# Optimization experiments

Measured on AMD Instinct MI355X. Metric: run time of the kernel, lower is better.

Reference implementation:

```python
import jax, jax.numpy as jnp
import numpy as np

DIM = 384
NUM_HEADS = 12
WS = 8            # window_size
SS = 4            # shift_size
HEAD_DIM = DIM // NUM_HEADS
SCALE = HEAD_DIM ** -0.5
N = WS * WS       # tokens per window
EPS = 1e-5
MLP_HIDDEN = 4 * DIM

# relative position index (static, matches torch buffer construction)
_coords = np.stack(np.meshgrid(np.arange(WS), np.arange(WS), indexing='ij')).reshape(2, -1)
_rel = (_coords[:, :, None] - _coords[:, None, :]).transpose(1, 2, 0)  # [N,N,2]
_rel[..., 0] += WS - 1
_rel[..., 1] += WS - 1
_rel[..., 0] *= 2 * WS - 1
RPI = jnp.asarray(_rel.sum(-1))  # [N,N] int


def layer_norm(x, g, b):
    m = x.mean(-1, keepdims=True)
    v = ((x - m) ** 2).mean(-1, keepdims=True)
    return (x - m) / jnp.sqrt(v + EPS) * g + b


def window_partition(x):
    B, Hh, Ww, C = x.shape
    x = x.reshape(B, Hh // WS, WS, Ww // WS, WS, C).transpose(0, 1, 3, 2, 4, 5)
    return x.reshape(-1, WS, WS, C)


def window_reverse(w, Hh, Ww):
    B = w.shape[0] // ((Hh // WS) * (Ww // WS))
    x = w.reshape(B, Hh // WS, Ww // WS, WS, WS, -1).transpose(0, 1, 3, 2, 4, 5)
    return x.reshape(B, Hh, Ww, -1)


def attention_mask(Hp, Wp):
    # region id along each axis: 0 = [0, Hp-WS), 1 = [Hp-WS, Hp-SS), 2 = [Hp-SS, Hp)
    h_id = np.zeros(Hp, np.int32); h_id[Hp - WS:Hp - SS] = 1; h_id[Hp - SS:] = 2
    w_id = np.zeros(Wp, np.int32); w_id[Wp - WS:Wp - SS] = 1; w_id[Wp - SS:] = 2
    cnt = h_id[:, None] * 3 + w_id[None, :]                      # [Hp, Wp]
    img = jnp.asarray(cnt, jnp.float32).reshape(1, Hp, Wp, 1)
    mw = window_partition(img).reshape(-1, N)                    # [nW, N]
    am = mw[:, None, :] - mw[:, :, None]                         # [nW, N, N]
    return jnp.where(am != 0, jnp.float32(-100.0), jnp.float32(0.0))


def setup_inputs() -> dict:
    key = jax.random.key(0)
    ks = jax.random.split(key, 8)
    B, H, W = 32, 64, 64
    std = 0.02
    return {
        'x': jax.random.normal(ks[0], (B, H * W, DIM), jnp.float32),
        'qkv_w': jax.random.normal(ks[1], (DIM, 3 * DIM), jnp.float32) * std,
        'qkv_b': jnp.zeros((3 * DIM,), jnp.float32),
        'proj_w': jax.random.normal(ks[2], (DIM, DIM), jnp.float32) * std,
        'proj_b': jnp.zeros((DIM,), jnp.float32),
        'rpb_table': jax.random.normal(ks[3], ((2 * WS - 1) * (2 * WS - 1), NUM_HEADS), jnp.float32) * std,
        'n1_g': jnp.ones((DIM,), jnp.float32), 'n1_b': jnp.zeros((DIM,), jnp.float32),
        'n2_g': jnp.ones((DIM,), jnp.float32), 'n2_b': jnp.zeros((DIM,), jnp.float32),
        'fc1_w': jax.random.normal(ks[4], (DIM, MLP_HIDDEN), jnp.float32) * std,
        'fc1_b': jnp.zeros((MLP_HIDDEN,), jnp.float32),
        'fc2_w': jax.random.normal(ks[5], (MLP_HIDDEN, DIM), jnp.float32) * std,
        'fc2_b': jnp.zeros((DIM,), jnp.float32),
        'H': 64, 'W': 64,
    }


def reference(x, qkv_w, qkv_b, proj_w, proj_b, rpb_table, n1_g, n1_b, n2_g, n2_b,
              fc1_w, fc1_b, fc2_w, fc2_b, H, W):
    B, L, C = x.shape
    shortcut = x
    h = layer_norm(x, n1_g, n1_b).reshape(B, H, W, C)
    pad_r = (WS - W % WS) % WS
    pad_b = (WS - H % WS) % WS
    if pad_r or pad_b:
        h = jnp.pad(h, ((0, 0), (0, pad_b), (0, pad_r), (0, 0)))
    Hp, Wp = H + pad_b, W + pad_r
    shifted = jnp.roll(h, shift=(-SS, -SS), axis=(1, 2))
    xw = window_partition(shifted).reshape(-1, N, C)             # [B_, N, C]
    B_ = xw.shape[0]

    qkv = (xw @ qkv_w + qkv_b).reshape(B_, N, 3, NUM_HEADS, HEAD_DIM)
    q = qkv[:, :, 0].transpose(0, 2, 1, 3) * SCALE               # [B_, h, N, d]
    k = qkv[:, :, 1].transpose(0, 2, 1, 3)
    v = qkv[:, :, 2].transpose(0, 2, 1, 3)

    attn = jnp.einsum('bhnd,bhmd->bhnm', q, k)                   # [B_, h, N, N]
    bias = rpb_table[RPI].transpose(2, 0, 1)                     # [h, N, N]
    attn = attn + bias[None]

    mask = attention_mask(Hp, Wp)                                # [nW, N, N]
    nW = mask.shape[0]
    attn = attn.reshape(B_ // nW, nW, NUM_HEADS, N, N) + mask[None, :, None]
    attn = jax.nn.softmax(attn.reshape(B_, NUM_HEADS, N, N), axis=-1)

    out = jnp.einsum('bhnm,bhmd->bhnd', attn, v)
    out = out.transpose(0, 2, 1, 3).reshape(B_, N, C)
    out = out @ proj_w + proj_b

    out = window_reverse(out.reshape(-1, WS, WS, C), Hp, Wp)
    out = jnp.roll(out, shift=(SS, SS), axis=(1, 2))
    out = out[:, :H, :W, :].reshape(B, H * W, C)

    x = shortcut + out
    h2 = layer_norm(x, n2_g, n2_b)
    mlp = jax.nn.gelu(h2 @ fc1_w + fc1_b, approximate=False) @ fc2_w + fc2_b
    return x + mlp
```

## Files before the change

### kernel.cpp

```cpp
#include <hip/hip_runtime.h>
#include <math.h>


#define ROWS_TOTAL 131072
#define NWIN_TOTAL 2048

typedef __attribute__((ext_vector_type(8))) __bf16 bf16x8;
typedef __attribute__((ext_vector_type(4))) float f32x4;
typedef __attribute__((ext_vector_type(8))) unsigned short ushort8;

__device__ __forceinline__ unsigned short f2bf(float f) {
  unsigned u = __builtin_bit_cast(unsigned, f);
  u = (u + 0x7fffu + ((u >> 16) & 1u)) >> 16;
  return (unsigned short)u;
}

__device__ __forceinline__ void gload16(const void* g, void* l) {
  __builtin_amdgcn_global_load_lds(
      (const __attribute__((address_space(1))) unsigned int*)g,
      (__attribute__((address_space(3))) unsigned int*)l, 16, 0, 0);
}

__device__ __forceinline__ int gather_row(int win, int t) {
  int b = win >> 6, wi = (win >> 3) & 7, wj = win & 7;
  int gi = (wi * 8 + (t >> 3) + 4) & 63;
  int gj = (wj * 8 + (t & 7) + 4) & 63;
  return (b << 12) + (gi << 6) + gj;
}

__device__ __forceinline__ void frag_mma(const ushort* As_, const ushort* Bs_,
                                         int wr, int wc, int lane,
                                         f32x4 acc[4][4]) {
  const int lk = (lane >> 4) * 8, lr = lane & 15;
  bf16x8 af[4], bfr[4];
#pragma unroll
  for (int mi = 0; mi < 4; ++mi)
    af[mi] = *(const bf16x8*)(As_ + (wr * 64 + mi * 16 + lr) * 32 + lk);
#pragma unroll
  for (int nj = 0; nj < 4; ++nj)
    bfr[nj] = *(const bf16x8*)(Bs_ + (wc * 64 + nj * 16 + lr) * 32 + lk);
#pragma unroll
  for (int mi = 0; mi < 4; ++mi)
#pragma unroll
    for (int nj = 0; nj < 4; ++nj)
      acc[mi][nj] = __builtin_amdgcn_mfma_f32_16x16x32_bf16(
          af[mi], bfr[nj], acc[mi][nj], 0, 0, 0);
}

__global__ __launch_bounds__(256) void wprep_k(
    const float* __restrict__ qkvw, const float* __restrict__ projw,
    const float* __restrict__ fc1w, const float* __restrict__ fc2w,
    ushort* __restrict__ wq, ushort* __restrict__ wp,
    ushort* __restrict__ w1, ushort* __restrict__ w2) {
  int gid = blockIdx.x * 256 + threadIdx.x;
  const int S1 = 1152 * 384;
  const int S2 = S1 + 384 * 384;
  const int S3 = S2 + 1536 * 384;
  const int S4 = S3 + 384 * 1536;
  if (gid < S1) {
    int n = gid / 384, k = gid - n * 384;
    wq[gid] = f2bf(qkvw[(size_t)k * 1152 + n]);
  } else if (gid < S2) {
    int i = gid - S1, n = i / 384, k = i - n * 384;
    wp[i] = f2bf(projw[(size_t)k * 384 + n]);
  } else if (gid < S3) {
    int i = gid - S2, n = i / 384, k = i - n * 384;
    w1[i] = f2bf(fc1w[(size_t)k * 1536 + n]);
  } else if (gid < S4) {
    int i = gid - S3, n = i / 1536, k = i - n * 1536;
    w2[i] = f2bf(fc2w[(size_t)k * 384 + n]);
  }
}

__global__ void ln_stats_k(const float* __restrict__ x, float* __restrict__ st) {
  int wid = threadIdx.x >> 6, lane = threadIdx.x & 63;
  int row = (blockIdx.x << 2) + wid;
  const float* p = x + (size_t)row * 384;
  float s = 0.f, ss = 0.f;
#pragma unroll
  for (int c = 0; c < 3; ++c) {
    float2 v = *(const float2*)(p + lane * 2 + c * 128);
    s += v.x + v.y;
    ss += v.x * v.x + v.y * v.y;
  }
#pragma unroll
  for (int o = 32; o > 0; o >>= 1) {
    s += __shfl_down(s, o);
    ss += __shfl_down(ss, o);
  }
  if (lane == 0) {
    float m = s * (1.f / 384.f);
    float var = ss * (1.f / 384.f) - m * m;
    *(float2*)(st + (size_t)row * 2) = make_float2(m, rsqrtf(var + 1e-5f));
  }
}

__global__ __launch_bounds__(256) void ln_apply_k(
    const float* __restrict__ x, const float* __restrict__ st,
    const float* __restrict__ g, const float* __restrict__ b,
    ushort* __restrict__ o) {
  int gid = blockIdx.x * 256 + threadIdx.x;
  int row = gid / 48, c8 = (gid - row * 48) * 8;
  float2 s2 = *(const float2*)(st + (size_t)row * 2);
  const float* xp = x + (size_t)row * 384 + c8;
  float4 v0 = *(const float4*)xp, v1 = *(const float4*)(xp + 4);
  float4 g0 = *(const float4*)(g + c8), g1 = *(const float4*)(g + c8 + 4);
  float4 b0 = *(const float4*)(b + c8), b1 = *(const float4*)(b + c8 + 4);
  float m = s2.x, r = s2.y;
  ushort8 w;
  w[0] = f2bf((v0.x - m) * r * g0.x + b0.x);
  w[1] = f2bf((v0.y - m) * r * g0.y + b0.y);
  w[2] = f2bf((v0.z - m) * r * g0.z + b0.z);
  w[3] = f2bf((v0.w - m) * r * g0.w + b0.w);
  w[4] = f2bf((v1.x - m) * r * g1.x + b1.x);
  w[5] = f2bf((v1.y - m) * r * g1.y + b1.y);
  w[6] = f2bf((v1.z - m) * r * g1.z + b1.z);
  w[7] = f2bf((v1.w - m) * r * g1.w + b1.w);
  *(ushort8*)(o + (size_t)row * 384 + c8) = w;
}

__global__ __launch_bounds__(256) void qkv_mfma_k(
    const ushort* __restrict__ xln, const ushort* __restrict__ wq,
    const float* __restrict__ qkvb, float* __restrict__ qd,
    float* __restrict__ kd, float* __restrict__ vd, int wc0) {
  __shared__ __align__(16) ushort As[2][4096];
  __shared__ __align__(16) ushort Bs[2][4096];
  __shared__ int rowS[128];
  const int tid = threadIdx.x;
  const int w = tid >> 6, lane = tid & 63;
  const int wr = w >> 1, wc = w & 1;
  const int bm = blockIdx.x, n0 = blockIdx.y * 128;
  if (tid < 128) {
    int win = wc0 + bm * 2 + (tid >> 6);
    rowS[tid] = gather_row(win, tid & 63);
  }
  __syncthreads();
  const int rA = w * 32 + (lane >> 2);
  const char* aS0 = (const char*)xln + (size_t)rowS[rA] * 768 + (lane & 3) * 16;
  const char* aS1 = (const char*)xln + (size_t)rowS[rA + 16] * 768 + (lane & 3) * 16;
  const char* bS0 = (const char*)wq + (size_t)(n0 + rA) * 768 + (lane & 3) * 16;
  const char* bS1 = (const char*)wq + (size_t)(n0 + rA + 16) * 768 + (lane & 3) * 16;
  f32x4 acc[4][4];
#pragma unroll
  for (int i = 0; i < 4; ++i)
#pragma unroll
    for (int j = 0; j < 4; ++j) acc[i][j] = (f32x4)(0.f);
  int cur = 0;
#define STG(B_, T_)                                   \
  { size_t ko = (size_t)(T_) * 64;                    \
    gload16(aS0 + ko, &As[B_][w * 1024]);             \
    gload16(aS1 + ko, &As[B_][w * 1024 + 512]);       \
    gload16(bS0 + ko, &Bs[B_][w * 1024]);             \
    gload16(bS1 + ko, &Bs[B_][w * 1024 + 512]); }
  STG(0, 0);
  __syncthreads();
  for (int t = 0; t < 11; ++t) {
    STG(cur ^ 1, t + 1);
    frag_mma(As[cur], Bs[cur], wr, wc, lane, acc);
    __syncthreads();
    cur ^= 1;
  }
  frag_mma(As[cur], Bs[cur], wr, wc, lane, acc);
#undef STG
  const float scale = 0.17677669529663687f;
#pragma unroll
  for (int mi = 0; mi < 4; ++mi) {
#pragma unroll
    for (int r = 0; r < 4; ++r) {
      int rr = wr * 64 + mi * 16 + ((lane >> 4) << 2) + r;
      int w_rel = bm * 2 + (rr >> 6), t = rr & 63;
#pragma unroll
      for (int nj = 0; nj < 4; ++nj) {
        int nc = n0 + wc * 64 + nj * 16 + (lane & 15);
        float v = acc[mi][nj][r] + qkvb[nc];
        int qi = nc / 384, rem = nc - qi * 384;
        int hh = rem >> 5, d = rem & 31;
        float* base = (qi == 0) ? qd : (qi == 1 ? kd : vd);
        if (qi == 0) v *= scale;
        base[(((size_t)w_rel * 12 + hh) << 11) + (t << 5) + d] = v;
      }
    }
  }
}

__global__ __launch_bounds__(128) void attn_k(
    const float* __restrict__ q, const float* __restrict__ k,
    const float* __restrict__ v, const float* __restrict__ rpb,
    ushort* __restrict__ ao, int wc0) {
  __shared__ __align__(16) float kbuf[2][64][32];
  __shared__ __align__(16) float vbuf[2][64][32];
  __shared__ float bias[2][232];
  __shared__ int region[64];
  const int tid = threadIdx.x;
  const int wid = tid >> 6, lane = tid & 63;
  const int w = blockIdx.x, win = wc0 + w;
  const int head = blockIdx.y * 2 + wid;
  if (tid < 64) {
    int wi = (win >> 3) & 7, wj = win & 7;
    int pi = wi * 8 + (tid >> 3), pj = wj * 8 + (tid & 7);
    int ri = pi < 56 ? 0 : (pi < 60 ? 1 : 2);
    int rj = pj < 56 ? 0 : (pj < 60 ? 1 : 2);
    region[tid] = ri * 3 + rj;
  }
  const size_t hb = ((size_t)w * 12 + head) * 2048;
  const float* kp = k + hb;
  const float* vp = v + hb;
#pragma unroll
  for (int s = 0; s < 8; ++s) {
    int f = s * 64 + lane;
    int r = f >> 3, c = (f & 7) << 2;
    *(float4*)&kbuf[wid][r][c] = *(const float4*)(kp + r * 32 + c);
    *(float4*)&vbuf[wid][r][c] = *(const float4*)(vp + r * 32 + c);
  }
  for (int s = lane; s < 225; s += 64) bias[wid][s] = rpb[s * 12 + head];
  __syncthreads();
  const int i = lane;
  float qr[32];
  const float* qp = q + hb + (i << 5);
#pragma unroll
  for (int c = 0; c < 32; c += 4) {
    float4 t4 = *(const float4*)(qp + c);
    qr[c] = t4.x; qr[c + 1] = t4.y; qr[c + 2] = t4.z; qr[c + 3] = t4.w;
  }
  const int yi = i >> 3, xi = i & 7, regi = region[i];
  float sc[64];
  float mx = -3.0e38f;
#pragma unroll
  for (int j = 0; j < 64; ++j) {
    float a = 0.f;
#pragma unroll
    for (int c = 0; c < 32; c += 4) {
      float4 kv = *(float4*)&kbuf[wid][j][c];
      a = fmaf(qr[c], kv.x, a);
      a = fmaf(qr[c + 1], kv.y, a);
      a = fmaf(qr[c + 2], kv.z, a);
      a = fmaf(qr[c + 3], kv.w, a);
    }
    int dy = yi - (j >> 3) + 7, dx = xi - (j & 7) + 7;
    a += bias[wid][dy * 15 + dx];
    if (region[j] != regi) a -= 100.f;
    sc[j] = a;
    mx = fmaxf(mx, a);
  }
  float sum = 0.f;
#pragma unroll
  for (int j = 0; j < 64; ++j) {
    float e = __expf(sc[j] - mx);
    sc[j] = e;
    sum += e;
  }
  const float inv = 1.f / sum;
  float o[32];
#pragma unroll
  for (int c = 0; c < 32; ++c) o[c] = 0.f;
#pragma unroll
  for (int j = 0; j < 64; ++j) {
    float p = sc[j];
#pragma unroll
    for (int c = 0; c < 32; c += 4) {
      float4 vv = *(float4*)&vbuf[wid][j][c];
      o[c] = fmaf(p, vv.x, o[c]);
      o[c + 1] = fmaf(p, vv.y, o[c + 1]);
      o[c + 2] = fmaf(p, vv.z, o[c + 2]);
      o[c + 3] = fmaf(p, vv.w, o[c + 3]);
    }
  }
  ushort* op = ao + ((size_t)(w * 64 + i)) * 384 + (head << 5);
#pragma unroll
  for (int c = 0; c < 32; c += 8) {
    ushort8 pk;
#pragma unroll
    for (int j2 = 0; j2 < 8; ++j2) pk[j2] = f2bf(o[c + j2] * inv);
    *(ushort8*)(op + c) = pk;
  }
}

__global__ __launch_bounds__(256) void proj_mfma_k(
    const ushort* __restrict__ ao, const ushort* __restrict__ wp,
    const float* __restrict__ pb, const float* __restrict__ x,
    float* __restrict__ x2, int wc0) {
  __shared__ __align__(16) ushort As[2][4096];
  __shared__ __align__(16) ushort Bs[2][4096];
  const int tid = threadIdx.x;
  const int w = tid >> 6, lane = tid & 63;
  const int wr = w >> 1, wc = w & 1;
  const int bm = blockIdx.x, n0 = blockIdx.y * 128;
  const int rA = w * 32 + (lane >> 2);
  const char* aS0 = (const char*)ao + (size_t)(bm * 128 + rA) * 768 + (lane & 3) * 16;
  const char* aS1 = aS0 + (size_t)16 * 768;
  const char* bS0 = (const char*)wp + (size_t)(n0 + rA) * 768 + (lane & 3) * 16;
  const char* bS1 = bS0 + (size_t)16 * 768;
  f32x4 acc[4][4];
#pragma unroll
  for (int i = 0; i < 4; ++i)
#pragma unroll
    for (int j = 0; j < 4; ++j) acc[i][j] = (f32x4)(0.f);
  int cur = 0;
#define STG(B_, T_)                                   \
  { size_t ko = (size_t)(T_) * 64;                    \
    gload16(aS0 + ko, &As[B_][w * 1024]);             \
    gload16(aS1 + ko, &As[B_][w * 1024 + 512]);       \
    gload16(bS0 + ko, &Bs[B_][w * 1024]);             \
    gload16(bS1 + ko, &Bs[B_][w * 1024 + 512]); }
  STG(0, 0);
  __syncthreads();
  for (int t = 0; t < 11; ++t) {
    STG(cur ^ 1, t + 1);
    frag_mma(As[cur], Bs[cur], wr, wc, lane, acc);
    __syncthreads();
    cur ^= 1;
  }
  frag_mma(As[cur], Bs[cur], wr, wc, lane, acc);
#undef STG
#pragma unroll
  for (int mi = 0; mi < 4; ++mi) {
#pragma unroll
    for (int r = 0; r < 4; ++r) {
      int rr = wr * 64 + mi * 16 + ((lane >> 4) << 2) + r;
      int lw = (bm * 128 + rr) >> 6, t = rr & 63;
      int gr = gather_row(wc0 + lw, t);
#pragma unroll
      for (int nj = 0; nj < 4; ++nj) {
        int nc = n0 + wc * 64 + nj * 16 + (lane & 15);
        size_t idx = (size_t)gr * 384 + nc;
        x2[idx] = acc[mi][nj][r] + pb[nc] + x[idx];
      }
    }
  }
}

__global__ __launch_bounds__(256) void fc1_mfma_k(
    const ushort* __restrict__ x2ln, const ushort* __restrict__ w1,
    const float* __restrict__ fb, ushort* __restrict__ hm, int row0) {
  __shared__ __align__(16) ushort As[2][4096];
  __shared__ __align__(16) ushort Bs[2][4096];
  const int tid = threadIdx.x;
  const int w = tid >> 6, lane = tid & 63;
  const int wr = w >> 1, wc = w & 1;
  const int bm = blockIdx.x, n0 = blockIdx.y * 128;
  const int rA = w * 32 + (lane >> 2);
  const char* aS0 = (const char*)x2ln + (size_t)(row0 + bm * 128 + rA) * 768 + (lane & 3) * 16;
  const char* aS1 = aS0 + (size_t)16 * 768;
  const char* bS0 = (const char*)w1 + (size_t)(n0 + rA) * 768 + (lane & 3) * 16;
  const char* bS1 = bS0 + (size_t)16 * 768;
  f32x4 acc[4][4];
#pragma unroll
  for (int i = 0; i < 4; ++i)
#pragma unroll
    for (int j = 0; j < 4; ++j) acc[i][j] = (f32x4)(0.f);
  int cur = 0;
#define STG(B_, T_)                                   \
  { size_t ko = (size_t)(T_) * 64;                    \
    gload16(aS0 + ko, &As[B_][w * 1024]);             \
    gload16(aS1 + ko, &As[B_][w * 1024 + 512]);       \
    gload16(bS0 + ko, &Bs[B_][w * 1024]);             \
    gload16(bS1 + ko, &Bs[B_][w * 1024 + 512]); }
  STG(0, 0);
  __syncthreads();
  for (int t = 0; t < 11; ++t) {
    STG(cur ^ 1, t + 1);
    frag_mma(As[cur], Bs[cur], wr, wc, lane, acc);
    __syncthreads();
    cur ^= 1;
  }
  frag_mma(As[cur], Bs[cur], wr, wc, lane, acc);
#undef STG
#pragma unroll
  for (int mi = 0; mi < 4; ++mi) {
#pragma unroll
    for (int r = 0; r < 4; ++r) {
      int rr = wr * 64 + mi * 16 + ((lane >> 4) << 2) + r;
      size_t lrow = (size_t)(bm * 128 + rr);
#pragma unroll
      for (int nj = 0; nj < 4; ++nj) {
        int nc = n0 + wc * 64 + nj * 16 + (lane & 15);
        float v = acc[mi][nj][r] + fb[nc];
        v = 0.5f * v * (1.f + erff(v * 0.70710678118654752f));
        hm[lrow * 1536 + nc] = f2bf(v);
      }
    }
  }
}

__global__ __launch_bounds__(256) void fc2_mfma_k(
    const ushort* __restrict__ hm, const ushort* __restrict__ w2,
    const float* __restrict__ fb, float* __restrict__ out, int row0) {
  __shared__ __align__(16) ushort As[2][4096];
  __shared__ __align__(16) ushort Bs[2][4096];
  const int tid = threadIdx.x;
  const int w = tid >> 6, lane = tid & 63;
  const int wr = w >> 1, wc = w & 1;
  const int bm = blockIdx.x, n0 = blockIdx.y * 128;
  const int rA = w * 32 + (lane >> 2);
  const char* aS0 = (const char*)hm + (size_t)(bm * 128 + rA) * 3072 + (lane & 3) * 16;
  const char* aS1 = aS0 + (size_t)16 * 3072;
  const char* bS0 = (const char*)w2 + (size_t)(n0 + rA) * 3072 + (lane & 3) * 16;
  const char* bS1 = bS0 + (size_t)16 * 3072;
  f32x4 acc[4][4];
#pragma unroll
  for (int i = 0; i < 4; ++i)
#pragma unroll
    for (int j = 0; j < 4; ++j) acc[i][j] = (f32x4)(0.f);
  int cur = 0;
#define STG(B_, T_)                                   \
  { size_t ko = (size_t)(T_) * 64;                    \
    gload16(aS0 + ko, &As[B_][w * 1024]);             \
    gload16(aS1 + ko, &As[B_][w * 1024 + 512]);       \
    gload16(bS0 + ko, &Bs[B_][w * 1024]);             \
    gload16(bS1 + ko, &Bs[B_][w * 1024 + 512]); }
  STG(0, 0);
  __syncthreads();
  for (int t = 0; t < 47; ++t) {
    STG(cur ^ 1, t + 1);
    frag_mma(As[cur], Bs[cur], wr, wc, lane, acc);
    __syncthreads();
    cur ^= 1;
  }
  frag_mma(As[cur], Bs[cur], wr, wc, lane, acc);
#undef STG
#pragma unroll
  for (int mi = 0; mi < 4; ++mi) {
#pragma unroll
    for (int r = 0; r < 4; ++r) {
      int rr = wr * 64 + mi * 16 + ((lane >> 4) << 2) + r;
      size_t grow = (size_t)(row0 + bm * 128 + rr);
#pragma unroll
      for (int nj = 0; nj < 4; ++nj) {
        int nc = n0 + wc * 64 + nj * 16 + (lane & 15);
        size_t idx = grow * 384 + nc;
        out[idx] = out[idx] + acc[mi][nj][r] + fb[nc];
      }
    }
  }
}

extern "C" void kernel_launch(void* const* d_in, const int* in_sizes, int n_in,
                              void* d_out, int out_size, void* d_ws, size_t ws_size,
                              hipStream_t stream) {
  const float* x = (const float*)d_in[0];
  const float* qkv_w = (const float*)d_in[1];
  const float* qkv_b = (const float*)d_in[2];
  const float* proj_w = (const float*)d_in[3];
  const float* proj_b = (const float*)d_in[4];
  const float* rpb = (const float*)d_in[5];
  const float* n1g = (const float*)d_in[6];
  const float* n1b = (const float*)d_in[7];
  const float* n2g = (const float*)d_in[8];
  const float* n2b = (const float*)d_in[9];
  const float* fc1w = (const float*)d_in[10];
  const float* fc1b = (const float*)d_in[11];
  const float* fc2w = (const float*)d_in[12];
  const float* fc2b = (const float*)d_in[13];
  float* out = (float*)d_out;
  char* ws = (char*)d_ws;

  float* st1 = (float*)ws;
  float* st2 = (float*)(ws + 1048576);
  ushort* wq = (ushort*)(ws + 2097152);
  ushort* wp = wq + 442368;
  ushort* w1 = wp + 147456;
  ushort* w2 = w1 + 589824;
  ushort* xln = (ushort*)(ws + 5636096);
  char* scratch = ws + 5636096 + 100663296;
  size_t base = 5636096 + 100663296;
  size_t ssz = (ws_size > base) ? ws_size - base : 0;

  wprep_k<<<6912, 256, 0, stream>>>(qkv_w, proj_w, fc1w, fc2w, wq, wp, w1, w2);
  ln_stats_k<<<ROWS_TOTAL / 4, 256, 0, stream>>>(x, st1);
  ln_apply_k<<<ROWS_TOTAL * 48 / 256, 256, 0, stream>>>(x, st1, n1g, n1b, xln);

  const size_t perwin = 344064;
  int nwc = (int)(ssz / perwin);
  if (nwc > NWIN_TOTAL) nwc = NWIN_TOTAL;
  nwc &= ~1;
  if (nwc < 2) nwc = 2;
  float* qd = (float*)scratch;
  float* kd = qd + (size_t)nwc * 24576;
  float* vd = kd + (size_t)nwc * 24576;
  ushort* ao = (ushort*)(vd + (size_t)nwc * 24576);
  for (int wc0 = 0; wc0 < NWIN_TOTAL; wc0 += nwc) {
    int nw = (NWIN_TOTAL - wc0 < nwc) ? (NWIN_TOTAL - wc0) : nwc;
    qkv_mfma_k<<<dim3(nw / 2, 9), 256, 0, stream>>>(xln, wq, qkv_b, qd, kd, vd, wc0);
    attn_k<<<dim3(nw, 6), 128, 0, stream>>>(qd, kd, vd, rpb, ao, wc0);
    proj_mfma_k<<<dim3(nw / 2, 3), 256, 0, stream>>>(ao, wp, proj_b, x, out, wc0);
  }

  ln_stats_k<<<ROWS_TOTAL / 4, 256, 0, stream>>>(out, st2);
  ln_apply_k<<<ROWS_TOTAL * 48 / 256, 256, 0, stream>>>(out, st2, n2g, n2b, xln);
  const size_t pergrp = 393216;
  int ngc = (int)(ssz / pergrp);
  if (ngc > 1024) ngc = 1024;
  if (ngc < 1) ngc = 1;
  ushort* hm = (ushort*)scratch;
  for (int g0 = 0; g0 < 1024; g0 += ngc) {
    int ng = (1024 - g0 < ngc) ? (1024 - g0) : ngc;
    fc1_mfma_k<<<dim3(ng, 12), 256, 0, stream>>>(xln, w1, fc1b, hm, g0 * 128);
    fc2_mfma_k<<<dim3(ng, 3), 256, 0, stream>>>(hm, w2, fc2b, out, g0 * 128);
  }
}
```

Baseline: 1.669 ms.

## Triple-buffer GEMM staging with swizzled LDS layout and explicit waitcnt barriers

Replaces the double-buffered K loop in all four MFMA GEMMs with a three-stage pipeline that keeps two tile loads in flight. It uses explicit vmcnt waits, sched barriers and raw s_barrier instead of __syncthreads, and raises wave priority around the MFMA block. It also XOR-swizzles the 16-byte chunk positions, applied on the global source side and on the fragment reads, to reduce LDS bank conflicts. The cost is 1.5x the LDS per block, which may lower occupancy, plus reliance on hand-placed wait counts being correct.

After: 1.574 ms. 1.06x faster.

```diff
diff --git a/kernel.cpp b/kernel.cpp
--- a/kernel.cpp
+++ b/kernel.cpp
@@ -31,14 +31,15 @@
 __device__ __forceinline__ void frag_mma(const ushort* As_, const ushort* Bs_,
                                          int wr, int wc, int lane,
                                          f32x4 acc[4][4]) {
-  const int lk = (lane >> 4) * 8, lr = lane & 15;
+  const int go = (((lane >> 4) ^ ((lane >> 1) & 3)) << 3);
+  const int lr = lane & 15;
   bf16x8 af[4], bfr[4];
 #pragma unroll
   for (int mi = 0; mi < 4; ++mi)
-    af[mi] = *(const bf16x8*)(As_ + (wr * 64 + mi * 16 + lr) * 32 + lk);
+    af[mi] = *(const bf16x8*)(As_ + (wr * 64 + mi * 16 + lr) * 32 + go);
 #pragma unroll
   for (int nj = 0; nj < 4; ++nj)
-    bfr[nj] = *(const bf16x8*)(Bs_ + (wc * 64 + nj * 16 + lr) * 32 + lk);
+    bfr[nj] = *(const bf16x8*)(Bs_ + (wc * 64 + nj * 16 + lr) * 32 + go);
 #pragma unroll
   for (int mi = 0; mi < 4; ++mi)
 #pragma unroll
@@ -46,6 +47,38 @@
       acc[mi][nj] = __builtin_amdgcn_mfma_f32_16x16x32_bf16(
           af[mi], bfr[nj], acc[mi][nj], 0, 0, 0);
 }
+
+#define VM4() asm volatile("s_waitcnt vmcnt(4)" ::: "memory")
+#define VM0() asm volatile("s_waitcnt vmcnt(0)" ::: "memory")
+#define SCB() __builtin_amdgcn_sched_barrier(0)
+#define BARR() __builtin_amdgcn_s_barrier()
+
+#define STG(B_, T_)                                   \
+  { size_t ko = (size_t)(T_) * 64;                    \
+    gload16(aS0 + ko, &As[B_][w * 1024]);             \
+    gload16(aS1 + ko, &As[B_][w * 1024 + 512]);       \
+    gload16(bS0 + ko, &Bs[B_][w * 1024]);             \
+    gload16(bS1 + ko, &Bs[B_][w * 1024 + 512]); }
+
+#define GEMM_PIPE(NK)                                               \
+  {                                                                 \
+    STG(0, 0);                                                      \
+    STG(1, 1);                                                      \
+    VM4(); SCB(); BARR(); SCB();                                    \
+    int cur = 0;                                                    \
+    for (int t = 0; t < (NK); ++t) {                                \
+      if (t + 2 < (NK)) {                                           \
+        int nb = cur + 2; if (nb >= 3) nb -= 3;                     \
+        STG(nb, t + 2);                                             \
+      }                                                             \
+      __builtin_amdgcn_s_setprio(1);                                \
+      frag_mma(&As[cur][0], &Bs[cur][0], wr, wc, lane, acc);        \
+      __builtin_amdgcn_s_setprio(0);                                \
+      if (t + 2 < (NK)) { VM4(); } else { VM0(); }                  \
+      SCB(); BARR(); SCB();                                         \
+      ++cur; if (cur == 3) cur = 0;                                 \
+    }                                                               \
+  }
 
 __global__ __launch_bounds__(256) void wprep_k(
     const float* __restrict__ qkvw, const float* __restrict__ projw,
@@ -123,8 +156,8 @@
     const ushort* __restrict__ xln, const ushort* __restrict__ wq,
     const float* __restrict__ qkvb, float* __restrict__ qd,
     float* __restrict__ kd, float* __restrict__ vd, int wc0) {
-  __shared__ __align__(16) ushort As[2][4096];
-  __shared__ __align__(16) ushort Bs[2][4096];
+  __shared__ __align__(16) ushort As[3][4096];
+  __shared__ __align__(16) ushort Bs[3][4096];
   __shared__ int rowS[128];
   const int tid = threadIdx.x;
   const int w = tid >> 6, lane = tid & 63;
@@ -136,32 +169,17 @@
   }
   __syncthreads();
   const int rA = w * 32 + (lane >> 2);
-  const char* aS0 = (const char*)xln + (size_t)rowS[rA] * 768 + (lane & 3) * 16;
-  const char* aS1 = (const char*)xln + (size_t)rowS[rA + 16] * 768 + (lane & 3) * 16;
-  const char* bS0 = (const char*)wq + (size_t)(n0 + rA) * 768 + (lane & 3) * 16;
-  const char* bS1 = (const char*)wq + (size_t)(n0 + rA + 16) * 768 + (lane & 3) * 16;
+  const int sle = (((lane & 3) ^ ((lane >> 3) & 3)) << 4);
+  const char* aS0 = (const char*)xln + (size_t)rowS[rA] * 768 + sle;
+  const char* aS1 = (const char*)xln + (size_t)rowS[rA + 16] * 768 + sle;
+  const char* bS0 = (const char*)wq + (size_t)(n0 + rA) * 768 + sle;
+  const char* bS1 = (const char*)wq + (size_t)(n0 + rA + 16) * 768 + sle;
   f32x4 acc[4][4];
 #pragma unroll
   for (int i = 0; i < 4; ++i)
 #pragma unroll
     for (int j = 0; j < 4; ++j) acc[i][j] = (f32x4)(0.f);
-  int cur = 0;
-#define STG(B_, T_)                                   \
-  { size_t ko = (size_t)(T_) * 64;                    \
-    gload16(aS0 + ko, &As[B_][w * 1024]);             \
-    gload16(aS1 + ko, &As[B_][w * 1024 + 512]);       \
-    gload16(bS0 + ko, &Bs[B_][w * 1024]);             \
-    gload16(bS1 + ko, &Bs[B_][w * 1024 + 512]); }
-  STG(0, 0);
-  __syncthreads();
-  for (int t = 0; t < 11; ++t) {
-    STG(cur ^ 1, t + 1);
-    frag_mma(As[cur], Bs[cur], wr, wc, lane, acc);
-    __syncthreads();
-    cur ^= 1;
-  }
-  frag_mma(As[cur], Bs[cur], wr, wc, lane, acc);
-#undef STG
+  GEMM_PIPE(12);
   const float scale = 0.17677669529663687f;
 #pragma unroll
   for (int mi = 0; mi < 4; ++mi) {
@@ -279,39 +297,24 @@
     const ushort* __restrict__ ao, const ushort* __restrict__ wp,
     const float* __restrict__ pb, const float* __restrict__ x,
     float* __restrict__ x2, int wc0) {
-  __shared__ __align__(16) ushort As[2][4096];
-  __shared__ __align__(16) ushort Bs[2][4096];
+  __shared__ __align__(16) ushort As[3][4096];
+  __shared__ __align__(16) ushort Bs[3][4096];
   const int tid = threadIdx.x;
   const int w = tid >> 6, lane = tid & 63;
   const int wr = w >> 1, wc = w & 1;
   const int bm = blockIdx.x, n0 = blockIdx.y * 128;
   const int rA = w * 32 + (lane >> 2);
-  const char* aS0 = (const char*)ao + (size_t)(bm * 128 + rA) * 768 + (lane & 3) * 16;
+  const int sle = (((lane & 3) ^ ((lane >> 3) & 3)) << 4);
+  const char* aS0 = (const char*)ao + (size_t)(bm * 128 + rA) * 768 + sle;
   const char* aS1 = aS0 + (size_t)16 * 768;
-  const char* bS0 = (const char*)wp + (size_t)(n0 + rA) * 768 + (lane & 3) * 16;
+  const char* bS0 = (const char*)wp + (size_t)(n0 + rA) * 768 + sle;
   const char* bS1 = bS0 + (size_t)16 * 768;
   f32x4 acc[4][4];
 #pragma unroll
   for (int i = 0; i < 4; ++i)
 #pragma unroll
     for (int j = 0; j < 4; ++j) acc[i][j] = (f32x4)(0.f);
-  int cur = 0;
-#define STG(B_, T_)                                   \
-  { size_t ko = (size_t)(T_) * 64;                    \
-    gload16(aS0 + ko, &As[B_][w * 1024]);             \
-    gload16(aS1 + ko, &As[B_][w * 1024 + 512]);       \
-    gload16(bS0 + ko, &Bs[B_][w * 1024]);             \
-    gload16(bS1 + ko, &Bs[B_][w * 1024 + 512]); }
-  STG(0, 0);
-  __syncthreads();
-  for (int t = 0; t < 11; ++t) {
-    STG(cur ^ 1, t + 1);
-    frag_mma(As[cur], Bs[cur], wr, wc, lane, acc);
-    __syncthreads();
-    cur ^= 1;
-  }
-  frag_mma(As[cur], Bs[cur], wr, wc, lane, acc);
-#undef STG
+  GEMM_PIPE(12);
 #pragma unroll
   for (int mi = 0; mi < 4; ++mi) {
 #pragma unroll
@@ -332,39 +335,25 @@
 __global__ __launch_bounds__(256) void fc1_mfma_k(
     const ushort* __restrict__ x2ln, const ushort* __restrict__ w1,
     const float* __restrict__ fb, ushort* __restrict__ hm, int row0) {
-  __shared__ __align__(16) ushort As[2][4096];
-  __shared__ __align__(16) ushort Bs[2][4096];
+  __shared__ __align__(16) ushort As[3][4096];
+  __shared__ __align__(16) ushort Bs[3][4096];
   const int tid = threadIdx.x;
   const int w = tid >> 6, lane = tid & 63;
   const int wr = w >> 1, wc = w & 1;
   const int bm = blockIdx.x, n0 = blockIdx.y * 128;
   const int rA = w * 32 + (lane >> 2);
-  const char* aS0 = (const char*)x2ln + (size_t)(row0 + bm * 128 + rA) * 768 + (lane & 3) * 16;
+  const int sle = (((lane & 3) ^ ((lane >> 3) & 3)) << 4);
+  const char* aS0 =
+      (const char*)x2ln + (size_t)(row0 + bm * 128 + rA) * 768 + sle;
   const char* aS1 = aS0 + (size_t)16 * 768;
-  const char* bS0 = (const char*)w1 + (size_t)(n0 + rA) * 768 + (lane & 3) * 16;
+  const char* bS0 = (const char*)w1 + (size_t)(n0 + rA) * 768 + sle;
   const char* bS1 = bS0 + (size_t)16 * 768;
   f32x4 acc[4][4];
 #pragma unroll
   for (int i = 0; i < 4; ++i)
 #pragma unroll
     for (int j = 0; j < 4; ++j) acc[i][j] = (f32x4)(0.f);
-  int cur = 0;
-#define STG(B_, T_)                                   \
-  { size_t ko = (size_t)(T_) * 64;                    \
-    gload16(aS0 + ko, &As[B_][w * 1024]);             \
-    gload16(aS1 + ko, &As[B_][w * 1024 + 512]);       \
-    gload16(bS0 + ko, &Bs[B_][w * 1024]);             \
-    gload16(bS1 + ko, &Bs[B_][w * 1024 + 512]); }
-  STG(0, 0);
-  __syncthreads();
-  for (int t = 0; t < 11; ++t) {
-    STG(cur ^ 1, t + 1);
-    frag_mma(As[cur], Bs[cur], wr, wc, lane, acc);
-    __syncthreads();
-    cur ^= 1;
-  }
-  frag_mma(As[cur], Bs[cur], wr, wc, lane, acc);
-#undef STG
+  GEMM_PIPE(12);
 #pragma unroll
   for (int mi = 0; mi < 4; ++mi) {
 #pragma unroll
@@ -385,39 +374,24 @@
 __global__ __launch_bounds__(256) void fc2_mfma_k(
     const ushort* __restrict__ hm, const ushort* __restrict__ w2,
     const float* __restrict__ fb, float* __restrict__ out, int row0) {
-  __shared__ __align__(16) ushort As[2][4096];
-  __shared__ __align__(16) ushort Bs[2][4096];
+  __shared__ __align__(16) ushort As[3][4096];
+  __shared__ __align__(16) ushort Bs[3][4096];
   const int tid = threadIdx.x;
   const int w = tid >> 6, lane = tid & 63;
   const int wr = w >> 1, wc = w & 1;
   const int bm = blockIdx.x, n0 = blockIdx.y * 128;
   const int rA = w * 32 + (lane >> 2);
-  const char* aS0 = (const char*)hm + (size_t)(bm * 128 + rA) * 3072 + (lane & 3) * 16;
+  const int sle = (((lane & 3) ^ ((lane >> 3) & 3)) << 4);
+  const char* aS0 = (const char*)hm + (size_t)(bm * 128 + rA) * 3072 + sle;
   const char* aS1 = aS0 + (size_t)16 * 3072;
-  const char* bS0 = (const char*)w2 + (size_t)(n0 + rA) * 3072 + (lane & 3) * 16;
+  const char* bS0 = (const char*)w2 + (size_t)(n0 + rA) * 3072 + sle;
   const char* bS1 = bS0 + (size_t)16 * 3072;
   f32x4 acc[4][4];
 #pragma unroll
   for (int i = 0; i < 4; ++i)
 #pragma unroll
     for (int j = 0; j < 4; ++j) acc[i][j] = (f32x4)(0.f);
-  int cur = 0;
-#define STG(B_, T_)                                   \
-  { size_t ko = (size_t)(T_) * 64;                    \
-    gload16(aS0 + ko, &As[B_][w * 1024]);             \
-    gload16(aS1 + ko, &As[B_][w * 1024 + 512]);       \
-    gload16(bS0 + ko, &Bs[B_][w * 1024]);             \
-    gload16(bS1 + ko, &Bs[B_][w * 1024 + 512]); }
-  STG(0, 0);
-  __syncthreads();
-  for (int t = 0; t < 47; ++t) {
-    STG(cur ^ 1, t + 1);
-    frag_mma(As[cur], Bs[cur], wr, wc, lane, acc);
-    __syncthreads();
-    cur ^= 1;
-  }
-  frag_mma(As[cur], Bs[cur], wr, wc, lane, acc);
-#undef STG
+  GEMM_PIPE(48);
 #pragma unroll
   for (int mi = 0; mi < 4; ++mi) {
 #pragma unroll
```
